# Performance work log

Measured on AMD Instinct MI355X. Metric: run time of the kernel, lower is better.

## Reference

```python
import jax, jax.numpy as jnp
import numpy as np

N, S, Q, P = 100000, 64, 50, 3  # pauli words, heads, qubits, pauli basis
EPS = 1e-12  # F.normalize clamp


def setup_inputs() -> dict:
    key = jax.random.key(0)
    k1, k2, k3, k4 = jax.random.split(key, 4)
    return {
        "batch_pauli_tensor": jax.random.uniform(k1, (N, Q, P), dtype=jnp.float32),
        "batch_coeff": jax.random.normal(k2, (N,), dtype=jnp.float32),
        "heads_param": jax.random.normal(k3, (S, Q, P), dtype=jnp.float32),
        "head_ratios_param": jax.random.normal(k4, (S,), dtype=jnp.float32),
    }


def reference(batch_pauli_tensor, batch_coeff, heads_param, head_ratios_param):
    s = heads_param.shape[0]
    heads = jax.nn.softplus(heads_param * 20.0)
    heads = heads / jnp.maximum(jnp.sum(heads, axis=-1, keepdims=True), EPS)
    hr = jax.nn.softplus(head_ratios_param * 20.0)
    hr = hr / jnp.maximum(jnp.sum(hr), EPS)
    hr = (hr + 0.001 / s) / 1.001
    # coverage: per-(word, head, qubit) match prob -> product over qubits -> ratio-weighted sum
    cov = jnp.einsum('nqp,sqp->nsq', batch_pauli_tensor, heads)  # [n, s, q]
    cov = jnp.prod(cov, axis=-1)                                 # [n, s]
    cov = jnp.einsum('s,ns->n', hr, cov)                         # [n]
    # variance loss
    return jnp.sum(batch_coeff ** 2 / cov)
```

## Files before the change

kernel.cpp:

```cpp
#include <hip/hip_runtime.h>
#include <math.h>

#define N_Q 50
#define N_P 3
#define N_S 64
#define ROW 150
#define BLK_ROWS 128
#define THREADS 256
#define SCHUNK 16

#define WS_CNT_OFF 6272
#define WS_HP_OFF 6336
#define WS_HRV_OFF 44736

__device__ __forceinline__ float softplus20(float x) {
    float z = x * 20.0f;
    return fmaxf(z, 0.0f) + log1pf(expf(-fabsf(z)));
}

__global__ void precompute_kernel(const float* __restrict__ heads_param,
                                  const float* __restrict__ hr_param,
                                  float* __restrict__ HP,
                                  float* __restrict__ hrv,
                                  int* __restrict__ cnt) {
    const int tid = threadIdx.x;
    if (blockIdx.x == 0) {
        if (tid == 0) *cnt = 0;
        if (tid < N_S) {
            float sp = softplus20(hr_param[tid]);
            float tot = sp;
            #pragma unroll
            for (int off = 32; off; off >>= 1) tot += __shfl_xor(tot, off);
            float hr = sp / fmaxf(tot, 1e-12f);
            hrv[tid] = (hr + 0.001f / (float)N_S) / 1.001f;
        }
    }
    int idx = blockIdx.x * blockDim.x + tid;
    if (idx < N_S * N_Q) {
        int q = idx / N_S;
        int s = idx - q * N_S;
        const float* hp = heads_param + ((size_t)s * N_Q + q) * N_P;
        float sp0 = softplus20(hp[0]);
        float sp1 = softplus20(hp[1]);
        float sp2 = softplus20(hp[2]);
        float denom = fmaxf(sp0 + sp1 + sp2, 1e-12f);
        float* o = HP + ((size_t)q * N_S + s) * 3;
        o[0] = sp0 / denom;
        o[1] = sp1 / denom;
        o[2] = sp2 / denom;
    }
}

__device__ __forceinline__ void computeQ2(const float4* __restrict__ Hq,
                                          float a0, float a1, float a2,
                                          float c0, float c1, float c2,
                                          float (&p)[SCHUNK], float (&p2)[SCHUNK]) {
    #pragma unroll
    for (int g = 0; g < 4; ++g) {
        float4 b0 = Hq[3 * g], b1 = Hq[3 * g + 1], b2 = Hq[3 * g + 2];
        p [4*g+0] *= fmaf(b0.x, a0, fmaf(b0.y, a1, b0.z * a2));
        p2[4*g+0] *= fmaf(b0.x, c0, fmaf(b0.y, c1, b0.z * c2));
        p [4*g+1] *= fmaf(b0.w, a0, fmaf(b1.x, a1, b1.y * a2));
        p2[4*g+1] *= fmaf(b0.w, c0, fmaf(b1.x, c1, b1.y * c2));
        p [4*g+2] *= fmaf(b1.z, a0, fmaf(b1.w, a1, b2.x * a2));
        p2[4*g+2] *= fmaf(b1.z, c0, fmaf(b1.w, c1, b2.x * c2));
        p [4*g+3] *= fmaf(b2.y, a0, fmaf(b2.z, a1, b2.w * a2));
        p2[4*g+3] *= fmaf(b2.y, c0, fmaf(b2.z, c1, b2.w * c2));
    }
}

__global__ __launch_bounds__(THREADS) void main_kernel(
    const float* __restrict__ A, const float* __restrict__ coeff,
    const float* __restrict__ HP, const float* __restrict__ hrv,
    double* __restrict__ partials, int* __restrict__ cnt,
    float* __restrict__ out, int N) {
    __shared__ float hHs[N_Q * N_S * 3];
    __shared__ float hrvl[N_S];
    __shared__ float covs[4][BLK_ROWS];
    __shared__ double redd[2];
    __shared__ int isLast;

    const int tid = threadIdx.x;
    const int lane = tid & 63;
    const int wave = tid >> 6;
    const int nbase = blockIdx.x * BLK_ROWS;

    for (int i = tid; i < (N_Q * N_S * 3) / 4; i += THREADS)
        ((float4*)hHs)[i] = ((const float4*)HP)[i];
    if (tid < N_S) hrvl[tid] = hrv[tid];
    __syncthreads();

    int n0 = nbase + lane;        if (n0 >= N) n0 = N - 1;
    int n1 = nbase + 64 + lane;   if (n1 >= N) n1 = N - 1;
    const float2* __restrict__ pA0 = (const float2*)A + (size_t)n0 * (ROW / 2);
    const float2* __restrict__ pA1 = (const float2*)A + (size_t)n1 * (ROW / 2);

    float prod0[SCHUNK], prod1[SCHUNK];
    #pragma unroll
    for (int i = 0; i < SCHUNK; ++i) { prod0[i] = 1.0f; prod1[i] = 1.0f; }

    const float4* __restrict__ Hbase = (const float4*)hHs + 12 * wave;

    #pragma unroll 5
    for (int w = 0; w < N_Q / 2; ++w) {
        float2 x0 = pA0[3 * w + 0], x1 = pA0[3 * w + 1], x2 = pA0[3 * w + 2];
        float2 y0 = pA1[3 * w + 0], y1 = pA1[3 * w + 1], y2 = pA1[3 * w + 2];
        const float4* Hq = Hbase + 96 * w;
        computeQ2(Hq,      x0.x, x0.y, x1.x,  y0.x, y0.y, y1.x, prod0, prod1);
        computeQ2(Hq + 48, x1.y, x2.x, x2.y,  y1.y, y2.x, y2.y, prod0, prod1);
    }

    float acc0 = 0.0f, acc1 = 0.0f;
    const int s0 = wave * SCHUNK;
    #pragma unroll
    for (int i = 0; i < SCHUNK; ++i) {
        float wgt = hrvl[s0 + i];
        acc0 = fmaf(wgt, prod0[i], acc0);
        acc1 = fmaf(wgt, prod1[i], acc1);
    }
    covs[wave][lane] = acc0;
    covs[wave][64 + lane] = acc1;
    __syncthreads();

    if (wave < 2) {
        const int row = wave * 64 + lane;
        const int n = nbase + row;
        float cov = covs[0][row] + covs[1][row] + covs[2][row] + covs[3][row];
        float term = 0.0f;
        if (n < N) { float c = coeff[n]; term = (c * c) / cov; }
        double td = (double)term;
        #pragma unroll
        for (int off = 32; off; off >>= 1) td += __shfl_down(td, off);
        if (lane == 0) redd[wave] = td;
    }
    __syncthreads();

    if (tid == 0) {
        partials[blockIdx.x] = redd[0] + redd[1];
        __threadfence();
        int v = atomicAdd(cnt, 1);
        isLast = (v == (int)gridDim.x - 1);
    }
    __syncthreads();

    if (isLast) {
        __threadfence();
        double s = 0.0;
        for (int i = tid; i < (int)gridDim.x; i += THREADS) s += partials[i];
        #pragma unroll
        for (int off = 32; off; off >>= 1) s += __shfl_down(s, off);
        __shared__ double redf[4];
        if (lane == 0) redf[wave] = s;
        __syncthreads();
        if (tid == 0) out[0] = (float)(redf[0] + redf[1] + redf[2] + redf[3]);
    }
}

extern "C" void kernel_launch(void* const* d_in, const int* in_sizes, int n_in,
                              void* d_out, int out_size, void* d_ws, size_t ws_size,
                              hipStream_t stream) {
    const float* A           = (const float*)d_in[0];
    const float* coeff       = (const float*)d_in[1];
    const float* heads_param = (const float*)d_in[2];
    const float* hr_param    = (const float*)d_in[3];
    const int N = in_sizes[1];
    const int nblocks = (N + BLK_ROWS - 1) / BLK_ROWS;

    char* ws = (char*)d_ws;
    double* partials = (double*)ws;
    int*   cnt = (int*)(ws + WS_CNT_OFF);
    float* HP  = (float*)(ws + WS_HP_OFF);
    float* hrv = (float*)(ws + WS_HRV_OFF);
    float* out = (float*)d_out;

    const int pre_blocks = (N_S * N_Q + THREADS - 1) / THREADS;
    precompute_kernel<<<pre_blocks, THREADS, 0, stream>>>(heads_param, hr_param,
                                                          HP, hrv, cnt);
    main_kernel<<<nblocks, THREADS, 0, stream>>>(A, coeff, HP, hrv, partials,
                                                 cnt, out, N);
}
```

Before: 154.1 us.

## Fuse head precompute into main kernel, use 8 waves, prefetch rows

```diff
diff --git a/kernel.cpp b/kernel.cpp
--- a/kernel.cpp
+++ b/kernel.cpp
@@ -6,49 +6,16 @@
 #define N_S 64
 #define ROW 150
 #define BLK_ROWS 128
-#define THREADS 256
-#define SCHUNK 16
+#define THREADS 512
+#define WAVES 8
+#define SCHUNK 8
+#define QPAD 196
 
 #define WS_CNT_OFF 6272
-#define WS_HP_OFF 6336
-#define WS_HRV_OFF 44736
 
 __device__ __forceinline__ float softplus20(float x) {
     float z = x * 20.0f;
     return fmaxf(z, 0.0f) + log1pf(expf(-fabsf(z)));
-}
-
-__global__ void precompute_kernel(const float* __restrict__ heads_param,
-                                  const float* __restrict__ hr_param,
-                                  float* __restrict__ HP,
-                                  float* __restrict__ hrv,
-                                  int* __restrict__ cnt) {
-    const int tid = threadIdx.x;
-    if (blockIdx.x == 0) {
-        if (tid == 0) *cnt = 0;
-        if (tid < N_S) {
-            float sp = softplus20(hr_param[tid]);
-            float tot = sp;
-            #pragma unroll
-            for (int off = 32; off; off >>= 1) tot += __shfl_xor(tot, off);
-            float hr = sp / fmaxf(tot, 1e-12f);
-            hrv[tid] = (hr + 0.001f / (float)N_S) / 1.001f;
-        }
-    }
-    int idx = blockIdx.x * blockDim.x + tid;
-    if (idx < N_S * N_Q) {
-        int q = idx / N_S;
-        int s = idx - q * N_S;
-        const float* hp = heads_param + ((size_t)s * N_Q + q) * N_P;
-        float sp0 = softplus20(hp[0]);
-        float sp1 = softplus20(hp[1]);
-        float sp2 = softplus20(hp[2]);
-        float denom = fmaxf(sp0 + sp1 + sp2, 1e-12f);
-        float* o = HP + ((size_t)q * N_S + s) * 3;
-        o[0] = sp0 / denom;
-        o[1] = sp1 / denom;
-        o[2] = sp2 / denom;
-    }
 }
 
 __device__ __forceinline__ void computeQ2(const float4* __restrict__ Hq,
@@ -56,7 +23,7 @@
                                           float c0, float c1, float c2,
                                           float (&p)[SCHUNK], float (&p2)[SCHUNK]) {
     #pragma unroll
-    for (int g = 0; g < 4; ++g) {
+    for (int g = 0; g < SCHUNK / 4; ++g) {
         float4 b0 = Hq[3 * g], b1 = Hq[3 * g + 1], b2 = Hq[3 * g + 2];
         p [4*g+0] *= fmaf(b0.x, a0, fmaf(b0.y, a1, b0.z * a2));
         p2[4*g+0] *= fmaf(b0.x, c0, fmaf(b0.y, c1, b0.z * c2));
@@ -69,15 +36,16 @@
     }
 }
 
-__global__ __launch_bounds__(THREADS) void main_kernel(
+__global__ __launch_bounds__(THREADS, 6) void main_kernel(
     const float* __restrict__ A, const float* __restrict__ coeff,
-    const float* __restrict__ HP, const float* __restrict__ hrv,
+    const float* __restrict__ heads_param, const float* __restrict__ hr_param,
     double* __restrict__ partials, int* __restrict__ cnt,
     float* __restrict__ out, int N) {
-    __shared__ float hHs[N_Q * N_S * 3];
+    __shared__ float hHs[N_Q * QPAD];
     __shared__ float hrvl[N_S];
-    __shared__ float covs[4][BLK_ROWS];
+    __shared__ float covs[WAVES][BLK_ROWS];
     __shared__ double redd[2];
+    __shared__ double redf[WAVES];
     __shared__ int isLast;
 
     const int tid = threadIdx.x;
@@ -85,9 +53,27 @@
     const int wave = tid >> 6;
     const int nbase = blockIdx.x * BLK_ROWS;
 
-    for (int i = tid; i < (N_Q * N_S * 3) / 4; i += THREADS)
-        ((float4*)hHs)[i] = ((const float4*)HP)[i];
-    if (tid < N_S) hrvl[tid] = hrv[tid];
+    if (tid < N_S) {
+        float sp = softplus20(hr_param[tid]);
+        float tot = sp;
+        #pragma unroll
+        for (int off = 32; off; off >>= 1) tot += __shfl_xor(tot, off);
+        float hr = sp / fmaxf(tot, 1e-12f);
+        hrvl[tid] = (hr + 0.001f / (float)N_S) / 1.001f;
+    }
+    for (int idx = tid; idx < N_S * N_Q; idx += THREADS) {
+        int s = idx / N_Q;
+        int q = idx - s * N_Q;
+        const float* hp = heads_param + (size_t)idx * N_P;
+        float sp0 = softplus20(hp[0]);
+        float sp1 = softplus20(hp[1]);
+        float sp2 = softplus20(hp[2]);
+        float denom = fmaxf(sp0 + sp1 + sp2, 1e-12f);
+        float* o = hHs + q * QPAD + s * 3;
+        o[0] = sp0 / denom;
+        o[1] = sp1 / denom;
+        o[2] = sp2 / denom;
+    }
     __syncthreads();
 
     int n0 = nbase + lane;        if (n0 >= N) n0 = N - 1;
@@ -99,15 +85,20 @@
     #pragma unroll
     for (int i = 0; i < SCHUNK; ++i) { prod0[i] = 1.0f; prod1[i] = 1.0f; }
 
-    const float4* __restrict__ Hbase = (const float4*)hHs + 12 * wave;
+    const float4* __restrict__ Hw = (const float4*)hHs + 6 * wave;
+
+    float2 x0 = pA0[0], x1 = pA0[1], x2 = pA0[2];
+    float2 y0 = pA1[0], y1 = pA1[1], y2 = pA1[2];
 
     #pragma unroll 5
     for (int w = 0; w < N_Q / 2; ++w) {
-        float2 x0 = pA0[3 * w + 0], x1 = pA0[3 * w + 1], x2 = pA0[3 * w + 2];
-        float2 y0 = pA1[3 * w + 0], y1 = pA1[3 * w + 1], y2 = pA1[3 * w + 2];
-        const float4* Hq = Hbase + 96 * w;
+        const int nb = (w < N_Q / 2 - 1) ? 3 * w + 3 : 0;
+        float2 nx0 = pA0[nb], nx1 = pA0[nb + 1], nx2 = pA0[nb + 2];
+        float2 ny0 = pA1[nb], ny1 = pA1[nb + 1], ny2 = pA1[nb + 2];
+        const float4* Hq = Hw + 98 * w;
         computeQ2(Hq,      x0.x, x0.y, x1.x,  y0.x, y0.y, y1.x, prod0, prod1);
-        computeQ2(Hq + 48, x1.y, x2.x, x2.y,  y1.y, y2.x, y2.y, prod0, prod1);
+        computeQ2(Hq + 49, x1.y, x2.x, x2.y,  y1.y, y2.x, y2.y, prod0, prod1);
+        x0 = nx0; x1 = nx1; x2 = nx2; y0 = ny0; y1 = ny1; y2 = ny2;
     }
 
     float acc0 = 0.0f, acc1 = 0.0f;
@@ -125,7 +116,9 @@
     if (wave < 2) {
         const int row = wave * 64 + lane;
         const int n = nbase + row;
-        float cov = covs[0][row] + covs[1][row] + covs[2][row] + covs[3][row];
+        float cov = 0.0f;
+        #pragma unroll
+        for (int wv = 0; wv < WAVES; ++wv) cov += covs[wv][row];
         float term = 0.0f;
         if (n < N) { float c = coeff[n]; term = (c * c) / cov; }
         double td = (double)term;
@@ -149,10 +142,14 @@
         for (int i = tid; i < (int)gridDim.x; i += THREADS) s += partials[i];
         #pragma unroll
         for (int off = 32; off; off >>= 1) s += __shfl_down(s, off);
-        __shared__ double redf[4];
         if (lane == 0) redf[wave] = s;
         __syncthreads();
-        if (tid == 0) out[0] = (float)(redf[0] + redf[1] + redf[2] + redf[3]);
+        if (tid == 0) {
+            double t = 0.0;
+            #pragma unroll
+            for (int wv = 0; wv < WAVES; ++wv) t += redf[wv];
+            out[0] = (float)t;
+        }
     }
 }
 
@@ -169,13 +166,9 @@
     char* ws = (char*)d_ws;
     double* partials = (double*)ws;
     int*   cnt = (int*)(ws + WS_CNT_OFF);
-    float* HP  = (float*)(ws + WS_HP_OFF);
-    float* hrv = (float*)(ws + WS_HRV_OFF);
     float* out = (float*)d_out;
 
-    const int pre_blocks = (N_S * N_Q + THREADS - 1) / THREADS;
-    precompute_kernel<<<pre_blocks, THREADS, 0, stream>>>(heads_param, hr_param,
-                                                          HP, hrv, cnt);
-    main_kernel<<<nblocks, THREADS, 0, stream>>>(A, coeff, HP, hrv, partials,
-                                                 cnt, out, N);
+    hipMemsetAsync(cnt, 0, sizeof(int), stream);
+    main_kernel<<<nblocks, THREADS, 0, stream>>>(A, coeff, heads_param, hr_param,
+                                                 partials, cnt, out, N);
 }
```

After: 203.2 us. 31.9% more time.
